# Performance work log

Hardware: AMD Instinct MI355X
Metric: run time of the kernel (lower is better)

The kernel has to match this reference:

```python
import jax, jax.numpy as jnp
import numpy as np

B, S, V, H, NH, DFF, L, T = 16, 256, 30522, 768, 12, 3072, 12, 9
DH = H // NH
LN_EPS = 1e-12


def _ln(x, g, b):
    m = x.mean(-1, keepdims=True)
    v = ((x - m) ** 2).mean(-1, keepdims=True)
    return (x - m) * jax.lax.rsqrt(v + LN_EPS) * g + b


def setup_inputs() -> dict:
    key = jax.random.key(0)
    ks = jax.random.split(key, 20)
    n = lambda k, shp: jax.random.normal(k, shp, jnp.float32) * 0.02
    return {
        "x": jax.random.randint(ks[0], (B, S), 0, V),
        "target": jax.random.randint(ks[1], (B, S), 0, T),
        "word_emb": n(ks[2], (V, H)),
        "pos_emb": n(ks[3], (S, H)),
        "type_emb": n(ks[4], (2, H)),
        "emb_ln_g": jnp.ones((H,)), "emb_ln_b": jnp.zeros((H,)),
        "Wq": n(ks[5], (L, H, H)), "bq": jnp.zeros((L, H)),
        "Wk": n(ks[6], (L, H, H)), "bk": jnp.zeros((L, H)),
        "Wv": n(ks[7], (L, H, H)), "bv": jnp.zeros((L, H)),
        "Wo": n(ks[8], (L, H, H)), "bo": jnp.zeros((L, H)),
        "ln1_g": jnp.ones((L, H)), "ln1_b": jnp.zeros((L, H)),
        "W1": n(ks[9], (L, H, DFF)), "b1": jnp.zeros((L, DFF)),
        "W2": n(ks[10], (L, DFF, H)), "b2": jnp.zeros((L, H)),
        "ln2_g": jnp.ones((L, H)), "ln2_b": jnp.zeros((L, H)),
        "clf_W": n(ks[11], (H, T)), "clf_b": jnp.zeros((T,)),
        "crf_start": jax.random.uniform(ks[12], (T,), jnp.float32, -0.1, 0.1),
        "crf_trans": jax.random.uniform(ks[13], (T, T), jnp.float32, -0.1, 0.1),
        "crf_end": jax.random.uniform(ks[14], (T,), jnp.float32, -0.1, 0.1),
    }


def _forward(x, target, word_emb, pos_emb, type_emb, emb_ln_g, emb_ln_b,
             Wq, bq, Wk, bk, Wv, bv, Wo, bo, ln1_g, ln1_b,
             W1, b1, W2, b2, ln2_g, ln2_b, clf_W, clf_b,
             crf_start, crf_trans, crf_end):
    # ---- BERT-base encoder (post-LN), no attention mask (all tokens valid) ----
    h = _ln(word_emb[x] + pos_emb[None, :, :] + type_emb[0][None, None, :], emb_ln_g, emb_ln_b)
    scale = 1.0 / np.sqrt(DH).astype(np.float32)
    for l in range(L):
        q = (h @ Wq[l] + bq[l]).reshape(B, S, NH, DH)
        k = (h @ Wk[l] + bk[l]).reshape(B, S, NH, DH)
        v = (h @ Wv[l] + bv[l]).reshape(B, S, NH, DH)
        att = jax.nn.softmax(jnp.einsum('bqhd,bkhd->bhqk', q, k) * scale, axis=-1)
        ctx = jnp.einsum('bhqk,bkhd->bqhd', att, v).reshape(B, S, H)
        h = _ln(h + ctx @ Wo[l] + bo[l], ln1_g[l], ln1_b[l])
        ff = jax.nn.gelu(h @ W1[l] + b1[l], approximate=False) @ W2[l] + b2[l]
        h = _ln(h + ff, ln2_g[l], ln2_b[l])

    logits = h @ clf_W + clf_b  # [B,S,T] emissions

    # ---- CRF negative log-likelihood (torchcrf semantics, reduction='mean') ----
    mask = target > -1                      # [B,S] bool
    tags = jnp.where(mask, target, 0)
    bidx = jnp.arange(B)
    emit = jnp.take_along_axis(logits, tags[..., None], axis=-1)[..., 0]  # [B,S]

    # numerator: score of the gold path
    num = crf_start[tags[:, 0]] + emit[:, 0]
    trans = crf_trans[tags[:, :-1], tags[:, 1:]]                          # [B,S-1]
    num = num + jnp.sum((trans + emit[:, 1:]) * mask[:, 1:], axis=1)
    last = jnp.sum(mask.astype(jnp.int32), axis=1) - 1
    num = num + crf_end[tags[bidx, last]]

    # denominator: forward algorithm (logsumexp recurrence over time)
    alpha0 = crf_start[None, :] + logits[:, 0]                            # [B,T]

    def step(alpha, xs):
        em, m = xs                                                        # [B,T], [B]
        nxt = jax.nn.logsumexp(alpha[:, :, None] + crf_trans[None], axis=1) + em
        return jnp.where(m[:, None], nxt, alpha), None

    alpha, _ = jax.lax.scan(step, alpha0,
                            (jnp.swapaxes(logits[:, 1:], 0, 1),
                             jnp.swapaxes(mask[:, 1:], 0, 1)))
    denom = jax.nn.logsumexp(alpha + crf_end[None, :], axis=1)

    llh = num - denom
    return -jnp.mean(llh)  # model returns -loss where loss = mean log-likelihood


def reference(x, target, word_emb, pos_emb, type_emb, emb_ln_g, emb_ln_b,
              Wq, bq, Wk, bk, Wv, bv, Wo, bo, ln1_g, ln1_b,
              W1, b1, W2, b2, ln2_g, ln2_b, clf_W, clf_b,
              crf_start, crf_trans, crf_end):
    return _forward(x, target, word_emb, pos_emb, type_emb, emb_ln_g, emb_ln_b,
                    Wq, bq, Wk, bk, Wv, bv, Wo, bo, ln1_g, ln1_b,
                    W1, b1, W2, b2, ln2_g, ln2_b, clf_W, clf_b,
                    crf_start, crf_trans, crf_end)
```

## Files before the change

### kernel.cpp

```cpp
#include <hip/hip_runtime.h>
#include <math.h>

#define B 16
#define S 256
#define H 768
#define NH 12
#define DH 64
#define DFF 3072
#define L 12
#define T 9
#define M (B*S)
#define LN_EPS 1e-12f
#define QKVS (3*H)
#define NCH 16
#define MH ((size_t)M * H)

typedef __attribute__((ext_vector_type(8))) __bf16 bf16x8;
typedef __attribute__((ext_vector_type(8))) unsigned short u16x8;
typedef __attribute__((ext_vector_type(4))) unsigned short u16x4;
typedef __attribute__((ext_vector_type(4))) float f32x4;

__device__ __forceinline__ unsigned short f2bf(float f) {
    unsigned int u = __float_as_uint(f);
    unsigned int r = u + 0x7fffu + ((u >> 16) & 1u);
    return (unsigned short)(r >> 16);
}
__device__ __forceinline__ float bf2f(unsigned short h) {
    return __uint_as_float((unsigned int)h << 16);
}

__global__ void convT4_kernel(const float* __restrict__ Wq, const float* __restrict__ Wk,
                              const float* __restrict__ Wv, const float* __restrict__ Wo,
                              unsigned short* __restrict__ wqkvT, unsigned short* __restrict__ woT) {
    __shared__ float tile[32][33];
    const int z = blockIdx.z;
    const int which = z / L, layer = z - which * L;
    const float* Wp = (which == 0 ? Wq : which == 1 ? Wk : which == 2 ? Wv : Wo)
                      + (size_t)layer * H * H;
    unsigned short* Tp = (which < 3)
        ? wqkvT + (size_t)layer * 3 * H * H + (size_t)which * H * H
        : woT + (size_t)layer * H * H;
    const int n0 = blockIdx.x * 32, k0 = blockIdx.y * 32;
    const int tx = threadIdx.x, ty = threadIdx.y;
#pragma unroll
    for (int i = 0; i < 32; i += 8)
        tile[ty + i][tx] = Wp[(size_t)(k0 + ty + i) * H + n0 + tx];
    __syncthreads();
    {
        const int u = ty * 32 + tx;
        const int r = u >> 3, kq = (u & 7) << 2;
        u16x4 o;
#pragma unroll
        for (int j = 0; j < 4; ++j) o[j] = f2bf(tile[kq + j][r]);
        *(u16x4*)&Tp[(size_t)(n0 + r) * H + k0 + kq] = o;
    }
}

__global__ void convT_kernel(const float* __restrict__ W, unsigned short* __restrict__ WT,
                             int K, int N, size_t dstLayerStride) {
    __shared__ float tile[32][33];
    const int layer = blockIdx.z;
    const float* Wp = W + (size_t)layer * K * N;
    unsigned short* Tp = WT + (size_t)layer * dstLayerStride;
    const int n0 = blockIdx.x * 32, k0 = blockIdx.y * 32;
    const int tx = threadIdx.x, ty = threadIdx.y;
#pragma unroll
    for (int i = 0; i < 32; i += 8)
        tile[ty + i][tx] = Wp[(size_t)(k0 + ty + i) * N + n0 + tx];
    __syncthreads();
    {
        const int u = ty * 32 + tx;
        const int r = u >> 3, kq = (u & 7) << 2;
        u16x4 o;
#pragma unroll
        for (int j = 0; j < 4; ++j) o[j] = f2bf(tile[kq + j][r]);
        *(u16x4*)&Tp[(size_t)(n0 + r) * K + k0 + kq] = o;
    }
}

__global__ void biascat_kernel(const float* __restrict__ bq, const float* __restrict__ bk,
                               const float* __restrict__ bv, float* __restrict__ out) {
    int idx = blockIdx.x * 256 + threadIdx.x;
    if (idx >= L * QKVS) return;
    int l = idx / QKVS, c = idx % QKVS;
    float v = (c < H) ? bq[l * H + c] : (c < 2 * H) ? bk[l * H + c - H] : bv[l * H + c - 2 * H];
    out[idx] = v;
}

__global__ void embed_ln_kernel(const int* __restrict__ x,
                                const float* __restrict__ word_emb,
                                const float* __restrict__ pos_emb,
                                const float* __restrict__ type_emb,
                                const float* __restrict__ g,
                                const float* __restrict__ bta,
                                unsigned short* __restrict__ hb) {
    const int row = blockIdx.x;
    const int s = row % S;
    const int tok = x[row];
    const int t = threadIdx.x;
    const int c = t << 2;
    const float4 wv = *(const float4*)&word_emb[(size_t)tok * H + c];
    const float4 pv = *(const float4*)&pos_emb[s * H + c];
    const float4 tv = *(const float4*)&type_emb[c];
    float v[4] = {wv.x + pv.x + tv.x, wv.y + pv.y + tv.y, wv.z + pv.z + tv.z, wv.w + pv.w + tv.w};
    float s1 = v[0] + v[1] + v[2] + v[3];
    float s2 = v[0]*v[0] + v[1]*v[1] + v[2]*v[2] + v[3]*v[3];
#pragma unroll
    for (int o = 32; o; o >>= 1) { s1 += __shfl_xor(s1, o); s2 += __shfl_xor(s2, o); }
    __shared__ float ws[3][2];
    const int w = t >> 6, l = t & 63;
    if (l == 0) { ws[w][0] = s1; ws[w][1] = s2; }
    __syncthreads();
    const float S1 = ws[0][0] + ws[1][0] + ws[2][0];
    const float S2 = ws[0][1] + ws[1][1] + ws[2][1];
    const float mean = S1 * (1.0f / H);
    const float var = fmaxf(S2 * (1.0f / H) - mean * mean, 0.f);
    const float inv = rsqrtf(var + LN_EPS);
    const float4 gv = *(const float4*)&g[c];
    const float4 bv = *(const float4*)&bta[c];
    u16x4 ob;
    ob[0] = f2bf((v[0] - mean) * inv * gv.x + bv.x);
    ob[1] = f2bf((v[1] - mean) * inv * gv.y + bv.y);
    ob[2] = f2bf((v[2] - mean) * inv * gv.z + bv.z);
    ob[3] = f2bf((v[3] - mean) * inv * gv.w + bv.w);
    *(u16x4*)&hb[(size_t)row * H + c] = ob;
}

template<int NS>
__global__ void residual_ln_kernel(unsigned short* __restrict__ hb,
                                   const unsigned short* __restrict__ delta,
                                   const float* __restrict__ g,
                                   const float* __restrict__ bta) {
    const int row = blockIdx.x;
    const int t = threadIdx.x;
    const int c = t << 2;
    const size_t base = (size_t)row * H + c;
    const u16x4 hv4 = *(const u16x4*)&hb[base];
    float v[4] = {bf2f(hv4[0]), bf2f(hv4[1]), bf2f(hv4[2]), bf2f(hv4[3])};
#pragma unroll
    for (int sgm = 0; sgm < NS; ++sgm) {
        const u16x4 dv4 = *(const u16x4*)&delta[sgm * MH + base];
#pragma unroll
        for (int j = 0; j < 4; ++j) v[j] += bf2f(dv4[j]);
    }
    float s1 = v[0] + v[1] + v[2] + v[3];
    float s2 = v[0]*v[0] + v[1]*v[1] + v[2]*v[2] + v[3]*v[3];
#pragma unroll
    for (int o = 32; o; o >>= 1) { s1 += __shfl_xor(s1, o); s2 += __shfl_xor(s2, o); }
    __shared__ float ws[3][2];
    const int w = t >> 6, l = t & 63;
    if (l == 0) { ws[w][0] = s1; ws[w][1] = s2; }
    __syncthreads();
    const float S1 = ws[0][0] + ws[1][0] + ws[2][0];
    const float S2 = ws[0][1] + ws[1][1] + ws[2][1];
    const float mean = S1 * (1.0f / H);
    const float var = fmaxf(S2 * (1.0f / H) - mean * mean, 0.f);
    const float inv = rsqrtf(var + LN_EPS);
    const float4 gv = *(const float4*)&g[c];
    const float4 bv = *(const float4*)&bta[c];
    u16x4 ob;
    ob[0] = f2bf((v[0] - mean) * inv * gv.x + bv.x);
    ob[1] = f2bf((v[1] - mean) * inv * gv.y + bv.y);
    ob[2] = f2bf((v[2] - mean) * inv * gv.z + bv.z);
    ob[3] = f2bf((v[3] - mean) * inv * gv.w + bv.w);
    *(u16x4*)&hb[base] = ob;
}

#define LSTR 72

template<int ACT, int MR, int NR>
__global__ __launch_bounds__(256, 3)
void gemm_bf16(const unsigned short* __restrict__ A,
               const unsigned short* __restrict__ WT,
               const float* __restrict__ bias,
               unsigned short* __restrict__ Cb,
               int Ksub, int Kfull, int N, size_t splitStride) {
    __shared__ unsigned short lA[MR * 32 * LSTR];
    __shared__ unsigned short lB[NR * 32 * LSTR];
    const int tid = threadIdx.x;
    const int z = blockIdx.z;
    const int gx = gridDim.x;
    const int nb = gx * gridDim.y;
    int f = blockIdx.y * gx + blockIdx.x;
    f = (f & 7) * (nb >> 3) + (f >> 3);
    const int m0 = (f / gx) * (MR * 32), n0 = (f % gx) * (NR * 32);
    const int l = tid & 63, w = tid >> 6;
    const int wr = w >> 1, wc = w & 1;
    const int lr = l & 15, kg = l >> 4;

    const int srow = tid >> 3, scol = (tid & 7) << 3;
    const int kOff = z * Ksub;
    const unsigned short* gA = A + (size_t)(m0 + srow) * Kfull + kOff + scol;
    const unsigned short* gB = WT + (size_t)(n0 + srow) * Kfull + kOff + scol;

    f32x4 acc[MR][NR];
#pragma unroll
    for (int i = 0; i < MR; ++i)
#pragma unroll
        for (int j = 0; j < NR; ++j) acc[i][j] = (f32x4){0.f, 0.f, 0.f, 0.f};

    u16x8 ra[MR], rb[NR];
#pragma unroll
    for (int p = 0; p < MR; ++p) ra[p] = *(const u16x8*)(gA + (size_t)p * 32 * Kfull);
#pragma unroll
    for (int p = 0; p < NR; ++p) rb[p] = *(const u16x8*)(gB + (size_t)p * 32 * Kfull);

    for (int kt = 0; kt < Ksub; kt += 64) {
#pragma unroll
        for (int p = 0; p < MR; ++p)
            *(u16x8*)&lA[(srow + p * 32) * LSTR + scol] = ra[p];
#pragma unroll
        for (int p = 0; p < NR; ++p)
            *(u16x8*)&lB[(srow + p * 32) * LSTR + scol] = rb[p];
        __syncthreads();
        if (kt + 64 < Ksub) {
#pragma unroll
            for (int p = 0; p < MR; ++p) ra[p] = *(const u16x8*)(gA + (size_t)p * 32 * Kfull + kt + 64);
#pragma unroll
            for (int p = 0; p < NR; ++p) rb[p] = *(const u16x8*)(gB + (size_t)p * 32 * Kfull + kt + 64);
        }
#pragma unroll
        for (int ks = 0; ks < 2; ++ks) {
            bf16x8 af[MR], bfr[NR];
#pragma unroll
            for (int m = 0; m < MR; ++m)
                af[m] = *(const bf16x8*)&lA[(wr * (MR * 16) + (m << 4) + lr) * LSTR + ks * 32 + (kg << 3)];
#pragma unroll
            for (int n = 0; n < NR; ++n)
                bfr[n] = *(const bf16x8*)&lB[((wc * (NR * 16)) + (n << 4) + lr) * LSTR + ks * 32 + (kg << 3)];
#pragma unroll
            for (int m = 0; m < MR; ++m)
#pragma unroll
                for (int n = 0; n < NR; ++n)
                    acc[m][n] = __builtin_amdgcn_mfma_f32_16x16x32_bf16(af[m], bfr[n], acc[m][n], 0, 0, 0);
        }
        __syncthreads();
    }

    unsigned short* Cz = Cb + (size_t)z * splitStride;
    const int rbase = m0 + wr * (MR * 16) + (kg << 2);
    const int cbase = n0 + wc * (NR * 16) + lr;
#pragma unroll
    for (int m = 0; m < MR; ++m) {
#pragma unroll
        for (int n = 0; n < NR; ++n) {
            const int col = cbase + (n << 4);
            const float bv = (z == 0) ? bias[col] : 0.f;
#pragma unroll
            for (int j = 0; j < 4; ++j) {
                const int row = rbase + (m << 4) + j;
                float v = acc[m][n][j] + bv;
                if (ACT == 1) v = 0.5f * v * (1.0f + erff(v * 0.70710678118654752440f));
                Cz[(size_t)row * N + col] = f2bf(v);
            }
        }
    }
}

__global__ __launch_bounds__(256, 2)
void attn_mfma(const unsigned short* __restrict__ qkv,
               unsigned short* __restrict__ ctxb) {
    __shared__ unsigned short Ks[256 * 72];
    __shared__ unsigned short Vt[64 * 264];
    __shared__ unsigned short Ps[4][16 * 72];

    int f = blockIdx.x;
    f = (f & 7) * 48 + (f >> 3);
    const int half = f & 1;
    const int hh = (f >> 1) % NH;
    const int b = f / (2 * NH);
    const int t = threadIdx.x;
    const int l = t & 63, w = t >> 6;
    const int l15 = l & 15, g = l >> 4;

    {
        const int c0 = (t & 7) << 3;
        int r = t >> 3;
#pragma unroll
        for (int it = 0; it < 8; ++it, r += 32) {
            u16x8 kv = *(const u16x8*)&qkv[(size_t)(b * S + r) * QKVS + H + hh * 64 + c0];
            *(u16x8*)&Ks[r * 72 + c0] = kv;
        }
    }
    {
        const int d0 = (t & 7) << 3;
        int s = t >> 3;
#pragma unroll
        for (int it = 0; it < 8; ++it, s += 32) {
            u16x8 vv = *(const u16x8*)&qkv[(size_t)(b * S + s) * QKVS + 2 * H + hh * 64 + d0];
#pragma unroll
            for (int j = 0; j < 8; ++j) {
                int d = d0 + j;
                Vt[d * 264 + (s ^ (((d >> 3) & 7) << 3))] = vv[j];
            }
        }
    }
    __syncthreads();

    unsigned short* ps = Ps[w];
#pragma unroll
    for (int qi = 0; qi < 2; ++qi) {
        const int qrow = half * 128 + qi * 64 + w * 16 + l15;
        const unsigned short* qp = &qkv[(size_t)(b * S + qrow) * QKVS + hh * 64 + g * 8];
        bf16x8 aq0 = *(const bf16x8*)qp;
        bf16x8 aq1 = *(const bf16x8*)(qp + 32);

        f32x4 acc[16];
#pragma unroll
        for (int n = 0; n < 16; ++n) acc[n] = (f32x4){0.f, 0.f, 0.f, 0.f};
        __builtin_amdgcn_s_setprio(1);
#pragma unroll
        for (int n = 0; n < 16; ++n) {
            const unsigned short* kp = &Ks[(n * 16 + l15) * 72 + g * 8];
            bf16x8 b0 = *(const bf16x8*)kp;
            bf16x8 b1 = *(const bf16x8*)(kp + 32);
            acc[n] = __builtin_amdgcn_mfma_f32_16x16x32_bf16(aq0, b0, acc[n], 0, 0, 0);
            acc[n] = __builtin_amdgcn_mfma_f32_16x16x32_bf16(aq1, b1, acc[n], 0, 0, 0);
        }
        __builtin_amdgcn_s_setprio(0);

        float inv[4];
#pragma unroll
        for (int j = 0; j < 4; ++j) {
            float mx = acc[0][j];
#pragma unroll
            for (int n = 1; n < 16; ++n) mx = fmaxf(mx, acc[n][j]);
            mx = fmaxf(mx, __shfl_xor(mx, 1));
            mx = fmaxf(mx, __shfl_xor(mx, 2));
            mx = fmaxf(mx, __shfl_xor(mx, 4));
            mx = fmaxf(mx, __shfl_xor(mx, 8));
            float sum = 0.f;
#pragma unroll
            for (int n = 0; n < 16; ++n) {
                float e = exp2f((acc[n][j] - mx) * 0.18033688011112042f);
                acc[n][j] = e;
                sum += e;
            }
            sum += __shfl_xor(sum, 1);
            sum += __shfl_xor(sum, 2);
            sum += __shfl_xor(sum, 4);
            sum += __shfl_xor(sum, 8);
            inv[j] = 1.0f / sum;
        }

        f32x4 cacc[4];
#pragma unroll
        for (int nd = 0; nd < 4; ++nd) cacc[nd] = (f32x4){0.f, 0.f, 0.f, 0.f};
#pragma unroll
        for (int c = 0; c < 4; ++c) {
#pragma unroll
            for (int nl = 0; nl < 4; ++nl) {
                int n = c * 4 + nl;
#pragma unroll
                for (int j = 0; j < 4; ++j)
                    ps[(g * 4 + j) * 72 + nl * 16 + l15] = f2bf(acc[n][j]);
            }
            bf16x8 pa0 = *(const bf16x8*)&ps[l15 * 72 + g * 8];
            bf16x8 pa1 = *(const bf16x8*)&ps[l15 * 72 + 32 + g * 8];
            __builtin_amdgcn_s_setprio(1);
#pragma unroll
            for (int nd = 0; nd < 4; ++nd) {
                const int d = nd * 16 + l15;
                const int swz = ((d >> 3) & 7) << 3;
                const unsigned short* vp0 = &Vt[d * 264 + ((c * 64 + g * 8) ^ swz)];
                const unsigned short* vp1 = &Vt[d * 264 + ((c * 64 + 32 + g * 8) ^ swz)];
                bf16x8 v0 = *(const bf16x8*)vp0;
                bf16x8 v1 = *(const bf16x8*)vp1;
                cacc[nd] = __builtin_amdgcn_mfma_f32_16x16x32_bf16(pa0, v0, cacc[nd], 0, 0, 0);
                cacc[nd] = __builtin_amdgcn_mfma_f32_16x16x32_bf16(pa1, v1, cacc[nd], 0, 0, 0);
            }
            __builtin_amdgcn_s_setprio(0);
        }

#pragma unroll
        for (int nd = 0; nd < 4; ++nd)
#pragma unroll
            for (int j = 0; j < 4; ++j) {
                int qr = half * 128 + qi * 64 + w * 16 + g * 4 + j;
                ctxb[(size_t)(b * S + qr) * H + hh * 64 + nd * 16 + l15] = f2bf(cacc[nd][j] * inv[j]);
            }
    }
}

__global__ void clf_kernel(const unsigned short* __restrict__ hb,
                           const float* __restrict__ W,
                           const float* __restrict__ bias,
                           float* __restrict__ logits) {
    const int row = blockIdx.x * 4 + (threadIdx.x >> 6);
    const int l = threadIdx.x & 63;
    const unsigned short* hp = hb + (size_t)row * H;
    float acc[T] = {};
#pragma unroll
    for (int i = 0; i < 12; ++i) {
        const int k = l + (i << 6);
        const float x = bf2f(hp[k]);
        const float* wp = &W[k * T];
#pragma unroll
        for (int n = 0; n < T; ++n) acc[n] += x * wp[n];
    }
#pragma unroll
    for (int o = 32; o; o >>= 1)
#pragma unroll
        for (int n = 0; n < T; ++n) acc[n] += __shfl_xor(acc[n], o);
    if (l < T) logits[(size_t)row * T + l] = acc[l] + bias[l];
}

__global__ void crf_chunk_kernel(const float* __restrict__ logits,
                                 const int* __restrict__ target,
                                 const float* __restrict__ trans,
                                 float* __restrict__ Tc) {
    const int blk = blockIdx.x;
    const int b = blk >> 4, c = blk & 15;
    const int t = threadIdx.x;
    const int i = t / 9, j = t - i * 9;
    const bool act = t < 81;
    __shared__ float Tb[2][81];
    const float* lg = logits + (size_t)b * S * T;
    const int* tg = target + b * S;
    const float K2 = 1.44269504088896340736f;
    const float IK = 0.69314718055994530942f;

    float trc[T];
    if (act) {
#pragma unroll
        for (int k = 0; k < T; ++k) trc[k] = trans[k * T + j];
        Tb[0][t] = (i == j) ? 0.f : -1e30f;
    }
    __syncthreads();

    int p = 0;
    const int s0 = c * 16 + 1;
    const int s1 = (c == 15) ? S : (s0 + 16);
    for (int s = s0; s < s1; ++s) {
        if (tg[s] > -1) {
            if (act) {
                const float em = lg[s * T + j];
                float v[T];
#pragma unroll
                for (int k = 0; k < T; ++k) v[k] = Tb[p][i * 9 + k] + trc[k];
                float mx = fmaxf(v[0], v[1]);
                mx = fmaxf(mx, fmaxf(v[2], v[3]));
                mx = fmaxf(mx, fmaxf(v[4], v[5]));
                mx = fmaxf(mx, fmaxf(v[6], v[7]));
                mx = fmaxf(mx, v[8]);
                float sum = 0.f;
#pragma unroll
                for (int k = 0; k < T; ++k) sum += exp2f((v[k] - mx) * K2);
                Tb[p ^ 1][t] = mx + IK * log2f(sum) + em;
            }
            __syncthreads();
            p ^= 1;
        }
    }
    if (act) Tc[(size_t)blk * 81 + t] = Tb[p][t];
}

__global__ __launch_bounds__(1024)
void crf_final_kernel(const float* __restrict__ logits,
                      const int* __restrict__ target,
                      const float* __restrict__ start,
                      const float* __restrict__ trans,
                      const float* __restrict__ endv,
                      const float* __restrict__ Tc,
                      float* __restrict__ out) {
    const int t = threadIdx.x;
    const int b = t >> 6, l = t & 63;
    const float* lg = logits + (size_t)b * S * T;
    const int* tg = target + b * S;
    const float K2 = 1.44269504088896340736f;
    const float IK = 0.69314718055994530942f;

    float pnum = 0.f; int pcnt = 0;
#pragma unroll
    for (int c = 0; c < 4; ++c) {
        const int s = 1 + l + (c << 6);
        if (s < S) {
            const int tcur = tg[s], tprev = tg[s - 1];
            const bool m = tcur > -1;
            const int tag = m ? tcur : 0;
            const int ptag = (tprev > -1) ? tprev : 0;
            if (m) { pnum += trans[ptag * T + tag] + lg[s * T + tag]; pcnt += 1; }
        }
    }
#pragma unroll
    for (int o = 32; o; o >>= 1) { pnum += __shfl_xor(pnum, o); pcnt += __shfl_xor(pcnt, o); }

    const int jj = (l < T) ? l : 0;
    float a = start[jj] + lg[jj];
    for (int c = 0; c < NCH; ++c) {
        const float* Tm = Tc + ((size_t)(b * NCH + c)) * 81;
        float v[T];
#pragma unroll
        for (int i2 = 0; i2 < T; ++i2) v[i2] = __shfl(a, i2) + Tm[i2 * 9 + jj];
        float mx = fmaxf(v[0], v[1]);
        mx = fmaxf(mx, fmaxf(v[2], v[3]));
        mx = fmaxf(mx, fmaxf(v[4], v[5]));
        mx = fmaxf(mx, fmaxf(v[6], v[7]));
        mx = fmaxf(mx, v[8]);
        float sum = 0.f;
#pragma unroll
        for (int k = 0; k < T; ++k) sum += exp2f((v[k] - mx) * K2);
        a = mx + IK * log2f(sum);
    }

    float val = (l < T) ? (a + endv[jj]) : -1e30f;
    float mx = val;
#pragma unroll
    for (int o = 8; o; o >>= 1) mx = fmaxf(mx, __shfl_xor(mx, o));
    float sm = (l < T) ? exp2f((val - mx) * K2) : 0.f;
#pragma unroll
    for (int o = 8; o; o >>= 1) sm += __shfl_xor(sm, o);
    const float denom = mx + IK * log2f(sm);

    __shared__ float part[16];
    if (l == 0) {
        const bool m0 = tg[0] > -1;
        const int tag0 = m0 ? tg[0] : 0;
        const int cnt = pcnt + (m0 ? 1 : 0);
        int lastIdx = cnt - 1; if (lastIdx < 0) lastIdx = 0;
        const int lt = tg[lastIdx];
        const int lastTag = (lt > -1) ? lt : 0;
        const float num = start[tag0] + lg[tag0] + pnum + endv[lastTag];
        part[b] = num - denom;
    }
    __syncthreads();
    if (t == 0) {
        float s = 0.f;
#pragma unroll
        for (int i = 0; i < 16; ++i) s += part[i];
        out[0] = -s * (1.0f / 16.0f);
    }
}

extern "C" void kernel_launch(void* const* d_in, const int* in_sizes, int n_in,
                              void* d_out, int out_size, void* d_ws, size_t ws_size,
                              hipStream_t stream) {
    const int*   x        = (const int*)d_in[0];
    const int*   target   = (const int*)d_in[1];
    const float* word_emb = (const float*)d_in[2];
    const float* pos_emb  = (const float*)d_in[3];
    const float* type_emb = (const float*)d_in[4];
    const float* emb_ln_g = (const float*)d_in[5];
    const float* emb_ln_b = (const float*)d_in[6];
    const float* Wq = (const float*)d_in[7];
    const float* bq = (const float*)d_in[8];
    const float* Wk = (const float*)d_in[9];
    const float* bk = (const float*)d_in[10];
    const float* Wv = (const float*)d_in[11];
    const float* bv = (const float*)d_in[12];
    const float* Wo = (const float*)d_in[13];
    const float* bo = (const float*)d_in[14];
    const float* ln1_g = (const float*)d_in[15];
    const float* ln1_b = (const float*)d_in[16];
    const float* W1 = (const float*)d_in[17];
    const float* b1 = (const float*)d_in[18];
    const float* W2 = (const float*)d_in[19];
    const float* b2 = (const float*)d_in[20];
    const float* ln2_g = (const float*)d_in[21];
    const float* ln2_b = (const float*)d_in[22];
    const float* clf_W = (const float*)d_in[23];
    const float* clf_b = (const float*)d_in[24];
    const float* crf_start = (const float*)d_in[25];
    const float* crf_trans = (const float*)d_in[26];
    const float* crf_end   = (const float*)d_in[27];

    char* ws = (char*)d_ws;
    size_t off = 0;
    auto alloc = [&](size_t bytes) { void* p = ws + off; off += (bytes + 255) & ~255ull; return p; };

    unsigned short* wqkvT = (unsigned short*)alloc((size_t)L * 3 * H * H * 2);
    unsigned short* woT   = (unsigned short*)alloc((size_t)L * H * H * 2);
    unsigned short* w1T   = (unsigned short*)alloc((size_t)L * H * DFF * 2);
    unsigned short* w2T   = (unsigned short*)alloc((size_t)L * H * DFF * 2);
    float*          bcat  = (float*)alloc((size_t)L * QKVS * 4);
    unsigned short* hb    = (unsigned short*)alloc(MH * 2);
    unsigned short* qkvb  = (unsigned short*)alloc((size_t)M * QKVS * 2);
    unsigned short* ctxb  = (unsigned short*)alloc(MH * 2);
    unsigned short* gob   = (unsigned short*)alloc(4 * MH * 2);
    unsigned short* ffb   = (unsigned short*)alloc((size_t)M * DFF * 2);
    float*          logits = (float*)alloc((size_t)M * T * 4);
    float*          Tcbuf  = (float*)alloc((size_t)B * NCH * 81 * 4);

    dim3 tb(32, 8);
    convT4_kernel<<<dim3(H / 32, H / 32, 4 * L), tb, 0, stream>>>(Wq, Wk, Wv, Wo, wqkvT, woT);
    convT_kernel<<<dim3(DFF / 32, H / 32, L), tb, 0, stream>>>(W1, w1T, H, DFF, (size_t)H * DFF);
    convT_kernel<<<dim3(H / 32, DFF / 32, L), tb, 0, stream>>>(W2, w2T, DFF, H, (size_t)H * DFF);
    biascat_kernel<<<(L * QKVS + 255) / 256, 256, 0, stream>>>(bq, bk, bv, bcat);

    embed_ln_kernel<<<M, 192, 0, stream>>>(x, word_emb, pos_emb, type_emb, emb_ln_g, emb_ln_b, hb);

    const dim3 gQKV(QKVS / 96, M / 128, 1);
    const dim3 gFF1(DFF / 128, M / 128, 1);
    const dim3 gWo (H / 128, M / 64, 2);
    const dim3 gFF2(H / 128, M / 64, 4);

    for (int l = 0; l < L; ++l) {
        gemm_bf16<0, 4, 3><<<gQKV, 256, 0, stream>>>(hb, wqkvT + (size_t)l * 3 * H * H, bcat + l * QKVS,
                                                     qkvb, H, H, QKVS, 0);
        attn_mfma<<<B * NH * 2, 256, 0, stream>>>(qkvb, ctxb);
        gemm_bf16<0, 2, 4><<<gWo, 256, 0, stream>>>(ctxb, woT + (size_t)l * H * H, bo + l * H,
                                                    gob, H / 2, H, H, MH);
        residual_ln_kernel<2><<<M, 192, 0, stream>>>(hb, gob, ln1_g + l * H, ln1_b + l * H);
        gemm_bf16<1, 4, 4><<<gFF1, 256, 0, stream>>>(hb, w1T + (size_t)l * H * DFF, b1 + l * DFF,
                                                     ffb, H, H, DFF, 0);
        gemm_bf16<0, 2, 4><<<gFF2, 256, 0, stream>>>(ffb, w2T + (size_t)l * H * DFF, b2 + l * H,
                                                     gob, DFF / 4, DFF, H, MH);
        residual_ln_kernel<4><<<M, 192, 0, stream>>>(hb, gob, ln2_g + l * H, ln2_b + l * H);
    }

    clf_kernel<<<M / 4, 256, 0, stream>>>(hb, clf_W, clf_b, logits);
    crf_chunk_kernel<<<B * NCH, 128, 0, stream>>>(logits, target, crf_trans, Tcbuf);
    crf_final_kernel<<<1, 1024, 0, stream>>>(logits, target, crf_start, crf_trans, crf_end, Tcbuf, (float*)d_out);
}
```

Before: 1.752 ms.

## Switch encoder GEMMs to FP8 e4m3 MFMA with scaled weights

Converts all weight matrices to e4m3 with a fixed scale of 64, and makes the LayerNorm, attention and FF1 outputs also emit FP8 copies of activations. The GEMMs use fp8 MFMA (16x16x32) with byte-sized LDS tiles and rescale the result in the epilogue. This halves operand bandwidth and LDS traffic and uses the faster FP8 matrix path. The cost is a large precision drop: e4m3 activations and weights with a static scale may hurt the accuracy of the final CRF loss.

```diff
diff --git a/kernel.cpp b/kernel.cpp
--- a/kernel.cpp
+++ b/kernel.cpp
@@ -19,6 +19,7 @@
 typedef __attribute__((ext_vector_type(8))) unsigned short u16x8;
 typedef __attribute__((ext_vector_type(4))) unsigned short u16x4;
 typedef __attribute__((ext_vector_type(4))) float f32x4;
+typedef __attribute__((ext_vector_type(4))) unsigned char u8x4;
 
 __device__ __forceinline__ unsigned short f2bf(float f) {
     unsigned int u = __float_as_uint(f);
@@ -28,18 +29,36 @@
 __device__ __forceinline__ float bf2f(unsigned short h) {
     return __uint_as_float((unsigned int)h << 16);
 }
+__device__ __forceinline__ unsigned char f2e4m3(float f) {
+    unsigned int u = __float_as_uint(f);
+    unsigned char s = (unsigned char)((u >> 24) & 0x80);
+    unsigned int a = u & 0x7FFFFFFFu;
+    if (a >= 0x43E00000u) return s | 0x7E;
+    if (a < 0x3C800000u) {
+        int q = (int)(__uint_as_float(a) * 512.0f + 0.5f);
+        if (q > 8) q = 8;
+        return s | (unsigned char)q;
+    }
+    unsigned int r = a + 0x7FFFFu + ((a >> 20) & 1u);
+    if (r >= 0x43E80000u) return s | 0x7E;
+    int e = (int)(r >> 23) - 127;
+    return s | (unsigned char)(((e + 7) << 3) | ((r >> 20) & 7));
+}
+
+#define WSCL 64.0f
+#define WINV 0.015625f
 
 __global__ void convT4_kernel(const float* __restrict__ Wq, const float* __restrict__ Wk,
                               const float* __restrict__ Wv, const float* __restrict__ Wo,
-                              unsigned short* __restrict__ wqkvT, unsigned short* __restrict__ woT) {
+                              unsigned char* __restrict__ wqkv8, unsigned char* __restrict__ wo8) {
     __shared__ float tile[32][33];
     const int z = blockIdx.z;
     const int which = z / L, layer = z - which * L;
     const float* Wp = (which == 0 ? Wq : which == 1 ? Wk : which == 2 ? Wv : Wo)
                       + (size_t)layer * H * H;
-    unsigned short* Tp = (which < 3)
-        ? wqkvT + (size_t)layer * 3 * H * H + (size_t)which * H * H
-        : woT + (size_t)layer * H * H;
+    unsigned char* Tp = (which < 3)
+        ? wqkv8 + (size_t)layer * 3 * H * H + (size_t)which * H * H
+        : wo8 + (size_t)layer * H * H;
     const int n0 = blockIdx.x * 32, k0 = blockIdx.y * 32;
     const int tx = threadIdx.x, ty = threadIdx.y;
 #pragma unroll
@@ -49,19 +68,19 @@
     {
         const int u = ty * 32 + tx;
         const int r = u >> 3, kq = (u & 7) << 2;
-        u16x4 o;
-#pragma unroll
-        for (int j = 0; j < 4; ++j) o[j] = f2bf(tile[kq + j][r]);
-        *(u16x4*)&Tp[(size_t)(n0 + r) * H + k0 + kq] = o;
-    }
-}
-
-__global__ void convT_kernel(const float* __restrict__ W, unsigned short* __restrict__ WT,
+        u8x4 o;
+#pragma unroll
+        for (int j = 0; j < 4; ++j) o[j] = f2e4m3(tile[kq + j][r] * WSCL);
+        *(u8x4*)&Tp[(size_t)(n0 + r) * H + k0 + kq] = o;
+    }
+}
+
+__global__ void convT_kernel(const float* __restrict__ W, unsigned char* __restrict__ W8,
                              int K, int N, size_t dstLayerStride) {
     __shared__ float tile[32][33];
     const int layer = blockIdx.z;
     const float* Wp = W + (size_t)layer * K * N;
-    unsigned short* Tp = WT + (size_t)layer * dstLayerStride;
+    unsigned char* Tp = W8 + (size_t)layer * dstLayerStride;
     const int n0 = blockIdx.x * 32, k0 = blockIdx.y * 32;
     const int tx = threadIdx.x, ty = threadIdx.y;
 #pragma unroll
@@ -71,10 +90,10 @@
     {
         const int u = ty * 32 + tx;
         const int r = u >> 3, kq = (u & 7) << 2;
-        u16x4 o;
-#pragma unroll
-        for (int j = 0; j < 4; ++j) o[j] = f2bf(tile[kq + j][r]);
-        *(u16x4*)&Tp[(size_t)(n0 + r) * K + k0 + kq] = o;
+        u8x4 o;
+#pragma unroll
+        for (int j = 0; j < 4; ++j) o[j] = f2e4m3(tile[kq + j][r] * WSCL);
+        *(u8x4*)&Tp[(size_t)(n0 + r) * K + k0 + kq] = o;
     }
 }
 
@@ -93,7 +112,8 @@
                                 const float* __restrict__ type_emb,
                                 const float* __restrict__ g,
                                 const float* __restrict__ bta,
-                                unsigned short* __restrict__ hb) {
+                                unsigned short* __restrict__ hb,
+                                unsigned char* __restrict__ hb8) {
     const int row = blockIdx.x;
     const int s = row % S;
     const int tok = x[row];
@@ -118,16 +138,19 @@
     const float inv = rsqrtf(var + LN_EPS);
     const float4 gv = *(const float4*)&g[c];
     const float4 bv = *(const float4*)&bta[c];
-    u16x4 ob;
-    ob[0] = f2bf((v[0] - mean) * inv * gv.x + bv.x);
-    ob[1] = f2bf((v[1] - mean) * inv * gv.y + bv.y);
-    ob[2] = f2bf((v[2] - mean) * inv * gv.z + bv.z);
-    ob[3] = f2bf((v[3] - mean) * inv * gv.w + bv.w);
+    float o0 = (v[0] - mean) * inv * gv.x + bv.x;
+    float o1 = (v[1] - mean) * inv * gv.y + bv.y;
+    float o2 = (v[2] - mean) * inv * gv.z + bv.z;
+    float o3 = (v[3] - mean) * inv * gv.w + bv.w;
+    u16x4 ob = {f2bf(o0), f2bf(o1), f2bf(o2), f2bf(o3)};
     *(u16x4*)&hb[(size_t)row * H + c] = ob;
+    u8x4 o8 = {f2e4m3(o0), f2e4m3(o1), f2e4m3(o2), f2e4m3(o3)};
+    *(u8x4*)&hb8[(size_t)row * H + c] = o8;
 }
 
 template<int NS>
 __global__ void residual_ln_kernel(unsigned short* __restrict__ hb,
+                                   unsigned char* __restrict__ hb8,
                                    const unsigned short* __restrict__ delta,
                                    const float* __restrict__ g,
                                    const float* __restrict__ bta) {
@@ -158,25 +181,28 @@
     const float inv = rsqrtf(var + LN_EPS);
     const float4 gv = *(const float4*)&g[c];
     const float4 bv = *(const float4*)&bta[c];
-    u16x4 ob;
-    ob[0] = f2bf((v[0] - mean) * inv * gv.x + bv.x);
-    ob[1] = f2bf((v[1] - mean) * inv * gv.y + bv.y);
-    ob[2] = f2bf((v[2] - mean) * inv * gv.z + bv.z);
-    ob[3] = f2bf((v[3] - mean) * inv * gv.w + bv.w);
+    float o0 = (v[0] - mean) * inv * gv.x + bv.x;
+    float o1 = (v[1] - mean) * inv * gv.y + bv.y;
+    float o2 = (v[2] - mean) * inv * gv.z + bv.z;
+    float o3 = (v[3] - mean) * inv * gv.w + bv.w;
+    u16x4 ob = {f2bf(o0), f2bf(o1), f2bf(o2), f2bf(o3)};
     *(u16x4*)&hb[base] = ob;
-}
-
-#define LSTR 72
-
-template<int ACT, int MR, int NR>
+    u8x4 o8 = {f2e4m3(o0), f2e4m3(o1), f2e4m3(o2), f2e4m3(o3)};
+    *(u8x4*)&hb8[base] = o8;
+}
+
+#define LSTR8 80
+
+template<int ACT, int MR, int NR, int OUT8>
 __global__ __launch_bounds__(256, 3)
-void gemm_bf16(const unsigned short* __restrict__ A,
-               const unsigned short* __restrict__ WT,
-               const float* __restrict__ bias,
-               unsigned short* __restrict__ Cb,
-               int Ksub, int Kfull, int N, size_t splitStride) {
-    __shared__ unsigned short lA[MR * 32 * LSTR];
-    __shared__ unsigned short lB[NR * 32 * LSTR];
+void gemm_fp8(const unsigned char* __restrict__ A,
+              const unsigned char* __restrict__ W8,
+              const float* __restrict__ bias,
+              unsigned short* __restrict__ Cb,
+              unsigned char* __restrict__ C8,
+              int Ksub, int Kfull, int N, size_t splitStride) {
+    __shared__ unsigned char lA[MR * 32 * LSTR8];
+    __shared__ unsigned char lB[NR * 32 * LSTR8];
     const int tid = threadIdx.x;
     const int z = blockIdx.z;
     const int gx = gridDim.x;
@@ -188,10 +214,12 @@
     const int wr = w >> 1, wc = w & 1;
     const int lr = l & 15, kg = l >> 4;
 
-    const int srow = tid >> 3, scol = (tid & 7) << 3;
+    const int srow = tid >> 2, scol = (tid & 3) << 4;
     const int kOff = z * Ksub;
-    const unsigned short* gA = A + (size_t)(m0 + srow) * Kfull + kOff + scol;
-    const unsigned short* gB = WT + (size_t)(n0 + srow) * Kfull + kOff + scol;
+    const unsigned char* gA = A + (size_t)(m0 + srow) * Kfull + kOff + scol;
+    const unsigned char* gB = W8 + (size_t)(n0 + srow) * Kfull + kOff + scol;
+    constexpr int PA = (MR * 32 + 63) / 64;
+    constexpr int PB = (NR * 32 + 63) / 64;
 
     f32x4 acc[MR][NR];
 #pragma unroll
@@ -199,45 +227,50 @@
 #pragma unroll
         for (int j = 0; j < NR; ++j) acc[i][j] = (f32x4){0.f, 0.f, 0.f, 0.f};
 
-    u16x8 ra[MR], rb[NR];
-#pragma unroll
-    for (int p = 0; p < MR; ++p) ra[p] = *(const u16x8*)(gA + (size_t)p * 32 * Kfull);
-#pragma unroll
-    for (int p = 0; p < NR; ++p) rb[p] = *(const u16x8*)(gB + (size_t)p * 32 * Kfull);
+    uint4 ra[PA], rb[PB];
+#pragma unroll
+    for (int p = 0; p < PA; ++p)
+        if (p * 64 + srow < MR * 32) ra[p] = *(const uint4*)(gA + (size_t)p * 64 * Kfull);
+#pragma unroll
+    for (int p = 0; p < PB; ++p)
+        if (p * 64 + srow < NR * 32) rb[p] = *(const uint4*)(gB + (size_t)p * 64 * Kfull);
 
     for (int kt = 0; kt < Ksub; kt += 64) {
 #pragma unroll
-        for (int p = 0; p < MR; ++p)
-            *(u16x8*)&lA[(srow + p * 32) * LSTR + scol] = ra[p];
-#pragma unroll
-        for (int p = 0; p < NR; ++p)
-            *(u16x8*)&lB[(srow + p * 32) * LSTR + scol] = rb[p];
+        for (int p = 0; p < PA; ++p)
+            if (p * 64 + srow < MR * 32)
+                *(uint4*)&lA[(p * 64 + srow) * LSTR8 + scol] = ra[p];
+#pragma unroll
+        for (int p = 0; p < PB; ++p)
+            if (p * 64 + srow < NR * 32)
+                *(uint4*)&lB[(p * 64 + srow) * LSTR8 + scol] = rb[p];
         __syncthreads();
         if (kt + 64 < Ksub) {
 #pragma unroll
-            for (int p = 0; p < MR; ++p) ra[p] = *(const u16x8*)(gA + (size_t)p * 32 * Kfull + kt + 64);
-#pragma unroll
-            for (int p = 0; p < NR; ++p) rb[p] = *(const u16x8*)(gB + (size_t)p * 32 * Kfull + kt + 64);
+            for (int p = 0; p < PA; ++p)
+                if (p * 64 + srow < MR * 32) ra[p] = *(const uint4*)(gA + (size_t)p * 64 * Kfull + kt + 64);
+#pragma unroll
+            for (int p = 0; p < PB; ++p)
+                if (p * 64 + srow < NR * 32) rb[p] = *(const uint4*)(gB + (size_t)p * 64 * Kfull + kt + 64);
         }
 #pragma unroll
         for (int ks = 0; ks < 2; ++ks) {
-            bf16x8 af[MR], bfr[NR];
+            long long af[MR], bfr[NR];
 #pragma unroll
             for (int m = 0; m < MR; ++m)
-                af[m] = *(const bf16x8*)&lA[(wr * (MR * 16) + (m << 4) + lr) * LSTR + ks * 32 + (kg << 3)];
+                af[m] = *(const long long*)&lA[(wr * (MR * 16) + (m << 4) + lr) * LSTR8 + ks * 32 + (kg << 3)];
 #pragma unroll
             for (int n = 0; n < NR; ++n)
-                bfr[n] = *(const bf16x8*)&lB[((wc * (NR * 16)) + (n << 4) + lr) * LSTR + ks * 32 + (kg << 3)];
+                bfr[n] = *(const long long*)&lB[(wc * (NR * 16) + (n << 4) + lr) * LSTR8 + ks * 32 + (kg << 3)];
 #pragma unroll
             for (int m = 0; m < MR; ++m)
 #pragma unroll
                 for (int n = 0; n < NR; ++n)
-                    acc[m][n] = __builtin_amdgcn_mfma_f32_16x16x32_bf16(af[m], bfr[n], acc[m][n], 0, 0, 0);
+                    acc[m][n] = __builtin_amdgcn_mfma_f32_16x16x32_fp8_fp8(af[m], bfr[n], acc[m][n], 0, 0, 0);
         }
         __syncthreads();
     }
 
-    unsigned short* Cz = Cb + (size_t)z * splitStride;
     const int rbase = m0 + wr * (MR * 16) + (kg << 2);
     const int cbase = n0 + wc * (NR * 16) + lr;
 #pragma unroll
@@ -249,9 +282,13 @@
 #pragma unroll
             for (int j = 0; j < 4; ++j) {
                 const int row = rbase + (m << 4) + j;
-                float v = acc[m][n][j] + bv;
+                float v = acc[m][n][j] * WINV + bv;
                 if (ACT == 1) v = 0.5f * v * (1.0f + erff(v * 0.70710678118654752440f));
-                Cz[(size_t)row * N + col] = f2bf(v);
+                if (OUT8) {
+                    C8[(size_t)z * splitStride + (size_t)row * N + col] = f2e4m3(v);
+                } else {
+                    Cb[(size_t)z * splitStride + (size_t)row * N + col] = f2bf(v);
+                }
             }
         }
     }
@@ -259,7 +296,7 @@
 
 __global__ __launch_bounds__(256, 2)
 void attn_mfma(const unsigned short* __restrict__ qkv,
-               unsigned short* __restrict__ ctxb) {
+               unsigned char* __restrict__ ctx8) {
     __shared__ unsigned short Ks[256 * 72];
     __shared__ unsigned short Vt[64 * 264];
     __shared__ unsigned short Ps[4][16 * 72];
@@ -377,7 +414,7 @@
 #pragma unroll
             for (int j = 0; j < 4; ++j) {
                 int qr = half * 128 + qi * 64 + w * 16 + g * 4 + j;
-                ctxb[(size_t)(b * S + qr) * H + hh * 64 + nd * 16 + l15] = f2bf(cacc[nd][j] * inv[j]);
+                ctx8[(size_t)(b * S + qr) * H + hh * 64 + nd * 16 + l15] = f2e4m3(cacc[nd][j] * inv[j]);
             }
     }
 }
@@ -568,26 +605,27 @@
     size_t off = 0;
     auto alloc = [&](size_t bytes) { void* p = ws + off; off += (bytes + 255) & ~255ull; return p; };
 
-    unsigned short* wqkvT = (unsigned short*)alloc((size_t)L * 3 * H * H * 2);
-    unsigned short* woT   = (unsigned short*)alloc((size_t)L * H * H * 2);
-    unsigned short* w1T   = (unsigned short*)alloc((size_t)L * H * DFF * 2);
-    unsigned short* w2T   = (unsigned short*)alloc((size_t)L * H * DFF * 2);
+    unsigned char*  wqkv8 = (unsigned char*)alloc((size_t)L * 3 * H * H);
+    unsigned char*  wo8   = (unsigned char*)alloc((size_t)L * H * H);
+    unsigned char*  w18   = (unsigned char*)alloc((size_t)L * H * DFF);
+    unsigned char*  w28   = (unsigned char*)alloc((size_t)L * H * DFF);
     float*          bcat  = (float*)alloc((size_t)L * QKVS * 4);
     unsigned short* hb    = (unsigned short*)alloc(MH * 2);
+    unsigned char*  hb8   = (unsigned char*)alloc(MH);
     unsigned short* qkvb  = (unsigned short*)alloc((size_t)M * QKVS * 2);
-    unsigned short* ctxb  = (unsigned short*)alloc(MH * 2);
+    unsigned char*  ctx8  = (unsigned char*)alloc(MH);
     unsigned short* gob   = (unsigned short*)alloc(4 * MH * 2);
-    unsigned short* ffb   = (unsigned short*)alloc((size_t)M * DFF * 2);
+    unsigned char*  ff8   = (unsigned char*)alloc((size_t)M * DFF);
     float*          logits = (float*)alloc((size_t)M * T * 4);
     float*          Tcbuf  = (float*)alloc((size_t)B * NCH * 81 * 4);
 
     dim3 tb(32, 8);
-    convT4_kernel<<<dim3(H / 32, H / 32, 4 * L), tb, 0, stream>>>(Wq, Wk, Wv, Wo, wqkvT, woT);
-    convT_kernel<<<dim3(DFF / 32, H / 32, L), tb, 0, stream>>>(W1, w1T, H, DFF, (size_t)H * DFF);
-    convT_kernel<<<dim3(H / 32, DFF / 32, L), tb, 0, stream>>>(W2, w2T, DFF, H, (size_t)H * DFF);
+    convT4_kernel<<<dim3(H / 32, H / 32, 4 * L), tb, 0, stream>>>(Wq, Wk, Wv, Wo, wqkv8, wo8);
+    convT_kernel<<<dim3(DFF / 32, H / 32, L), tb, 0, stream>>>(W1, w18, H, DFF, (size_t)H * DFF);
+    convT_kernel<<<dim3(H / 32, DFF / 32, L), tb, 0, stream>>>(W2, w28, DFF, H, (size_t)H * DFF);
     biascat_kernel<<<(L * QKVS + 255) / 256, 256, 0, stream>>>(bq, bk, bv, bcat);
 
-    embed_ln_kernel<<<M, 192, 0, stream>>>(x, word_emb, pos_emb, type_emb, emb_ln_g, emb_ln_b, hb);
+    embed_ln_kernel<<<M, 192, 0, stream>>>(x, word_emb, pos_emb, type_emb, emb_ln_g, emb_ln_b, hb, hb8);
 
     const dim3 gQKV(QKVS / 96, M / 128, 1);
     const dim3 gFF1(DFF / 128, M / 128, 1);
@@ -595,17 +633,17 @@
     const dim3 gFF2(H / 128, M / 64, 4);
 
     for (int l = 0; l < L; ++l) {
-        gemm_bf16<0, 4, 3><<<gQKV, 256, 0, stream>>>(hb, wqkvT + (size_t)l * 3 * H * H, bcat + l * QKVS,
-                                                     qkvb, H, H, QKVS, 0);
-        attn_mfma<<<B * NH * 2, 256, 0, stream>>>(qkvb, ctxb);
-        gemm_bf16<0, 2, 4><<<gWo, 256, 0, stream>>>(ctxb, woT + (size_t)l * H * H, bo + l * H,
-                                                    gob, H / 2, H, H, MH);
-        residual_ln_kernel<2><<<M, 192, 0, stream>>>(hb, gob, ln1_g + l * H, ln1_b + l * H);
-        gemm_bf16<1, 4, 4><<<gFF1, 256, 0, stream>>>(hb, w1T + (size_t)l * H * DFF, b1 + l * DFF,
-                                                     ffb, H, H, DFF, 0);
-        gemm_bf16<0, 2, 4><<<gFF2, 256, 0, stream>>>(ffb, w2T + (size_t)l * H * DFF, b2 + l * H,
-                                                     gob, DFF / 4, DFF, H, MH);
-        residual_ln_kernel<4><<<M, 192, 0, stream>>>(hb, gob, ln2_g + l * H, ln2_b + l * H);
+        gemm_fp8<0, 4, 3, 0><<<gQKV, 256, 0, stream>>>(hb8, wqkv8 + (size_t)l * 3 * H * H, bcat + l * QKVS,
+                                                       qkvb, nullptr, H, H, QKVS, 0);
+        attn_mfma<<<B * NH * 2, 256, 0, stream>>>(qkvb, ctx8);
+        gemm_fp8<0, 2, 4, 0><<<gWo, 256, 0, stream>>>(ctx8, wo8 + (size_t)l * H * H, bo + l * H,
+                                                      gob, nullptr, H / 2, H, H, MH);
+        residual_ln_kernel<2><<<M, 192, 0, stream>>>(hb, hb8, gob, ln1_g + l * H, ln1_b + l * H);
+        gemm_fp8<1, 4, 4, 1><<<gFF1, 256, 0, stream>>>(hb8, w18 + (size_t)l * H * DFF, b1 + l * DFF,
+                                                       nullptr, ff8, H, H, DFF, 0);
+        gemm_fp8<0, 2, 4, 0><<<gFF2, 256, 0, stream>>>(ff8, w28 + (size_t)l * H * DFF, b2 + l * H,
+                                                       gob, nullptr, DFF / 4, DFF, H, MH);
+        residual_ln_kernel<4><<<M, 192, 0, stream>>>(hb, hb8, gob, ln2_g + l * H, ln2_b + l * H);
     }
 
     clf_kernel<<<M / 4, 256, 0, stream>>>(hb, clf_W, clf_b, logits);
```

Measured after the change: 2.703 ms. 54.3% more time.
